# Performance work log

Measured on AMD Instinct MI355X. Metric: run time of the kernel, lower is better.

Reference implementation:

```python
import jax, jax.numpy as jnp
import numpy as np

BETA = 0.9
THRESHOLD = 1.0
SG_A = 0.5  # rectangular surrogate half-width
NUM_LAYERS = 4

@jax.custom_vjp
def spike(v):
    # heaviside fire on (mem - threshold)
    return (v > 0).astype(v.dtype)

def _spike_fwd(v):
    return spike(v), v

def _spike_bwd(v, g):
    # rectangular surrogate gradient: pass-through inside |v| <= a
    return (g * (jnp.abs(v) <= SG_A).astype(g.dtype),)

spike.defvjp(_spike_fwd, _spike_bwd)

def _lif(mem_prev, inp):
    # snntorch Leaky: reset from previous mem (detached), subtract mechanism
    reset = jax.lax.stop_gradient((mem_prev > THRESHOLD).astype(inp.dtype))
    mem = BETA * mem_prev + inp - reset * THRESHOLD
    spk = spike(mem - THRESHOLD)
    return spk, mem

def setup_inputs() -> dict:
    key = jax.random.key(0)
    k0, k1, k2 = jax.random.split(key, 3)
    L, N, OBS, H = 512, 256, 128, 512
    x = jax.random.normal(k0, (L, N, OBS), jnp.float32)
    mem0 = jnp.zeros((NUM_LAYERS + 1, N, H), jnp.float32)
    enc_W = jax.random.normal(k1, (H, OBS), jnp.float32) / np.sqrt(OBS).astype(np.float32)
    enc_b = jnp.zeros((H,), jnp.float32)
    fc_W = jax.random.normal(k2, (NUM_LAYERS, H, H), jnp.float32) / np.sqrt(H).astype(np.float32)
    fc_b = jnp.zeros((NUM_LAYERS, H), jnp.float32)
    return {"x": x, "mem0": mem0, "enc_W": enc_W, "enc_b": enc_b, "fc_W": fc_W, "fc_b": fc_b}

def reference(x, mem0, enc_W, enc_b, fc_W, fc_b):
    # x: [L, N, obs]; mem0: [num_layers+1, N, H]
    def step(mem_stack, x_t):
        spk, m0 = _lif(mem_stack[0], x_t @ enc_W.T + enc_b)  # encoder: Linear + LIF
        mems = [m0]
        for i in range(NUM_LAYERS):
            spk, m = _lif(mem_stack[i + 1], spk @ fc_W[i].T + fc_b[i])
            mems.append(m)
        return jnp.stack(mems), spk
    mem_final, outputs = jax.lax.scan(step, mem0, x)
    # outputs: [L, N, H] spikes of last layer per step; mem_final: final state list (stacked)
    return outputs, mem_final
```

## Files before the change

kernel.cpp:

```cpp
#include <hip/hip_runtime.h>

#define H 512
#define NB 256
#define OBS 128
#define LSTEPS 512
#define TB 8
#define NTB (LSTEPS / TB)
#define NPHASE (NTB + 8)
#define NWG 256
#define NTHR 512
#define NLDS_TT 5
#define PLANE (NB * H)
#define MPLANE ((size_t)TB * NB * 8)
typedef unsigned long long u64;

__global__ __launch_bounds__(256) void prep_weights(const float* __restrict__ enc_W,
                                                    const float* __restrict__ fc_W,
                                                    float* __restrict__ enc_Wt,
                                                    float* __restrict__ fc_Wt) {
    int idx = blockIdx.x * 256 + threadIdx.x;
    int stride = gridDim.x * 256;
    for (int i = idx; i < 4 * H * H; i += stride) {
        int l = i >> 18;
        int k = (i >> 9) & 511;
        int h = i & 511;
        fc_Wt[i] = fc_W[l * H * H + h * H + k];
    }
    for (int i = idx; i < OBS * H; i += stride) {
        int k = i >> 9;
        int h = i & 511;
        enc_Wt[i] = enc_W[h * OBS + k];
    }
}

__device__ __forceinline__ u64 spread2(unsigned int v) {
    u64 z = v;
    z = (z | (z << 16)) & 0x0000FFFF0000FFFFull;
    z = (z | (z << 8))  & 0x00FF00FF00FF00FFull;
    z = (z | (z << 4))  & 0x0F0F0F0F0F0F0F0Full;
    z = (z | (z << 2))  & 0x3333333333333333ull;
    z = (z | (z << 1))  & 0x5555555555555555ull;
    return z;
}
__device__ __forceinline__ u64 spread4(unsigned int v) {
    u64 z = v & 0xFFFFull;
    z = (z | (z << 24)) & 0x000000FF000000FFull;
    z = (z | (z << 12)) & 0x000F000F000F000Full;
    z = (z | (z << 6))  & 0x0303030303030303ull;
    z = (z | (z << 3))  & 0x1111111111111111ull;
    return z;
}

__global__ __launch_bounds__(NTHR, 2) void snn_persistent(
    const float* __restrict__ x,
    const float* __restrict__ mem0,
    const float* __restrict__ enc_b,
    const float* __restrict__ fc_b,
    const float* __restrict__ enc_Wt,
    const float* __restrict__ fc_Wt,
    u64* __restrict__ masks,
    int* __restrict__ bar,
    float* __restrict__ out)
{
    __shared__ float Wsh[513][64];
    __shared__ u64  Msh[TB][32][8];

    const int tid = threadIdx.x;
    const int wg  = blockIdx.x;
    const int wave = tid >> 6;
    const int lane = tid & 63;

    const int layer = wg >> 6;
    const int hs = (wg >> 3) & 7;
    const int g  = wg & 7;
    const int h0 = hs << 6;
    const int n0 = g << 5;
    const int ng = lane >> 4;
    const int hq = lane & 15;
    const int hq4 = hq << 2;
    const int nl = (wave << 2) | ng;

    const int ew  = wg >> 5;
    const int eh0 = ew << 6;
    const int en0 = (wg & 31) << 3;
    const int enl = 2 * wave + (lane >> 5);
    const int en  = en0 + enl;
    const int hp  = lane & 31;
    const int eh  = eh0 + 2 * hp;

    int* slots = bar;
    int* done  = bar + 256;
    int* rel   = bar + 288;
    const int grp = wg & 7;
    const int gidx = wg >> 3;

    const float* Wl = fc_Wt + (size_t)layer * H * H;
    #pragma unroll
    for (int i = 0; i < 16; ++i) {
        int id = tid + NTHR * i;
        int row = id >> 4, c4 = id & 15;
        *(float4*)&Wsh[row][c4 * 4] = *(const float4*)(Wl + (size_t)row * H + h0 + c4 * 4);
    }
    if (tid < 64) Wsh[512][tid] = 0.f;

    const float* WgBase = Wl + h0 + hq4;

    const float4 bfc = *(const float4*)(fc_b + layer * H + h0 + hq4);
    float4 mem_fc = *(const float4*)(mem0 + (size_t)(layer + 1) * PLANE +
                                     (size_t)(n0 + nl) * H + h0 + hq4);
    float2 be2 = make_float2(0.f, 0.f);
    float2 mem_e = make_float2(0.f, 0.f);
    if (wave < 4) {
        be2   = *(const float2*)(enc_b + eh);
        mem_e = *(const float2*)(mem0 + (size_t)en * H + eh);
    }

    __syncthreads();

    for (int p = 0; p < NPHASE; ++p) {
        const int  tb_fc  = p - 2 - 2 * layer;
        const bool fc_act = (tb_fc >= 0) && (tb_fc < NTB);
        const bool enc_act = (p < NTB);

        if (tid == 0 && p >= 2) {
            while (__hip_atomic_load(rel + grp * 32,
                                     __ATOMIC_RELAXED, __HIP_MEMORY_SCOPE_AGENT) < p - 1)
                __builtin_amdgcn_s_sleep(1);
        }
        __syncthreads();

        if (fc_act) {
            const u64* msrc = masks + ((size_t)layer * 4 + ((p + 2) & 3)) * MPLANE;
            #pragma unroll
            for (int i = 0; i < 4; ++i) {
                int id = tid + NTHR * i;
                int tt = id >> 8, n_l = (id >> 3) & 31, w = id & 7;
                u64 v = __hip_atomic_load(msrc + ((size_t)tt * NB + n0 + n_l) * 8 + w,
                                          __ATOMIC_RELAXED, __HIP_MEMORY_SCOPE_AGENT);
                Msh[tt][n_l][w] = v;
            }
        }
        __syncthreads();

        if (enc_act && wave < 4) {
            float2 ea[TB];
            #pragma unroll
            for (int tt = 0; tt < TB; ++tt) ea[tt] = make_float2(0.f, 0.f);
            const float* xbase = x + (size_t)(TB * p) * NB * OBS + (size_t)en * OBS;
            for (int k2 = 0; k2 < 64; ++k2) {
                float2 w0 = *(const float2*)(enc_Wt + (size_t)(2 * k2) * H + eh);
                float2 w1 = *(const float2*)(enc_Wt + (size_t)(2 * k2 + 1) * H + eh);
                #pragma unroll
                for (int tt = 0; tt < TB; ++tt) {
                    float2 xv = *(const float2*)(xbase + (size_t)tt * NB * OBS + 2 * k2);
                    ea[tt].x += xv.x * w0.x; ea[tt].y += xv.x * w0.y;
                    ea[tt].x += xv.y * w1.x; ea[tt].y += xv.y * w1.y;
                }
            }
            u64* edst = masks + (size_t)(0 * 4 + (p & 3)) * MPLANE;
            #pragma unroll
            for (int tt = 0; tt < TB; ++tt) {
                float m0, m1;
                {
                    float inp = ea[tt].x + be2.x; float mp = mem_e.x;
                    float reset = (mp > 1.0f) ? 1.0f : 0.0f;
                    m0 = 0.9f * mp + inp - reset; mem_e.x = m0;
                }
                {
                    float inp = ea[tt].y + be2.y; float mp = mem_e.y;
                    float reset = (mp > 1.0f) ? 1.0f : 0.0f;
                    m1 = 0.9f * mp + inp - reset; mem_e.y = m1;
                }
                u64 b0 = __ballot(m0 > 1.0f);
                u64 b1 = __ballot(m1 > 1.0f);
                unsigned int s0 = (unsigned int)(b0 >> (lane & 32));
                unsigned int s1 = (unsigned int)(b1 >> (lane & 32));
                u64 word = spread2(s0) | (spread2(s1) << 1);
                if ((lane & 31) == 0)
                    __hip_atomic_store(edst + ((size_t)tt * NB + en) * 8 + ew, word,
                                       __ATOMIC_RELAXED, __HIP_MEMORY_SCOPE_AGENT);
            }
        }

        if (fc_act) {
            float* outp = out + (size_t)(TB * tb_fc) * PLANE;
            u64* mdst = masks + ((size_t)(layer + 1) * 4 + (p & 3)) * MPLANE;

            #define LIF_PACK(TT, MNEW)                                                     \
            {                                                                              \
                if (layer < 3) {                                                           \
                    u64 B0 = __ballot(MNEW.x > 1.0f);                                      \
                    u64 B1 = __ballot(MNEW.y > 1.0f);                                      \
                    u64 B2 = __ballot(MNEW.z > 1.0f);                                      \
                    u64 B3 = __ballot(MNEW.w > 1.0f);                                      \
                    const int sh = ng << 4;                                                \
                    u64 word = spread4((unsigned int)(B0 >> sh))                           \
                             | (spread4((unsigned int)(B1 >> sh)) << 1)                    \
                             | (spread4((unsigned int)(B2 >> sh)) << 2)                    \
                             | (spread4((unsigned int)(B3 >> sh)) << 3);                   \
                    if (hq == 0)                                                           \
                        __hip_atomic_store(mdst + ((size_t)(TT) * NB + n0 + nl) * 8 + hs,  \
                                           word, __ATOMIC_RELAXED, __HIP_MEMORY_SCOPE_AGENT); \
                } else {                                                                   \
                    float4 s4;                                                             \
                    s4.x = (MNEW.x > 1.0f) ? 1.0f : 0.0f;                                  \
                    s4.y = (MNEW.y > 1.0f) ? 1.0f : 0.0f;                                  \
                    s4.z = (MNEW.z > 1.0f) ? 1.0f : 0.0f;                                  \
                    s4.w = (MNEW.w > 1.0f) ? 1.0f : 0.0f;                                  \
                    *(float4*)(outp + (size_t)(TT) * PLANE +                               \
                               (size_t)(n0 + nl) * H + h0 + hq4) = s4;                     \
                }                                                                          \
            }

            #define LIF_STEP(ACC, MNEW)                                                    \
                { float inp = ACC.x + bfc.x; float mp = mem_fc.x;                          \
                  float reset = (mp > 1.0f) ? 1.0f : 0.0f; MNEW.x = 0.9f * mp + inp - reset; } \
                { float inp = ACC.y + bfc.y; float mp = mem_fc.y;                          \
                  float reset = (mp > 1.0f) ? 1.0f : 0.0f; MNEW.y = 0.9f * mp + inp - reset; } \
                { float inp = ACC.z + bfc.z; float mp = mem_fc.z;                          \
                  float reset = (mp > 1.0f) ? 1.0f : 0.0f; MNEW.z = 0.9f * mp + inp - reset; } \
                { float inp = ACC.w + bfc.w; float mp = mem_fc.w;                          \
                  float reset = (mp > 1.0f) ? 1.0f : 0.0f; MNEW.w = 0.9f * mp + inp - reset; } \
                mem_fc = MNEW;

            #pragma unroll 1
            for (int tt = 0; tt < NLDS_TT; ++tt) {
                float4 acc = make_float4(0.f, 0.f, 0.f, 0.f);
                #pragma unroll 1
                for (int w = 0; w < 8; ++w) {
                    u64 rem = Msh[tt][nl][w];
                    if (!__any((int)(rem != 0ull))) continue;
                    const int kb = w << 6;
                    const int pop = __popcll(rem);
                    if (pop) {
                        const int nit = (pop + 1) >> 1;
                        int b0 = kb + __builtin_ctzll(rem); rem &= rem - 1;
                        int b1 = rem ? kb + __builtin_ctzll(rem) : 512; rem &= rem - 1;
                        float4 w0 = *(const float4*)&Wsh[b0][hq4];
                        float4 w1 = make_float4(0.f, 0.f, 0.f, 0.f);
                        if (b1 < 512) w1 = *(const float4*)&Wsh[b1][hq4];
                        #pragma unroll 1
                        for (int i = 1; i < nit; ++i) {
                            int c0 = kb + __builtin_ctzll(rem); rem &= rem - 1;
                            int c1 = rem ? kb + __builtin_ctzll(rem) : 512; rem &= rem - 1;
                            float4 u0 = *(const float4*)&Wsh[c0][hq4];
                            float4 u1 = make_float4(0.f, 0.f, 0.f, 0.f);
                            if (c1 < 512) u1 = *(const float4*)&Wsh[c1][hq4];
                            acc.x += w0.x; acc.y += w0.y; acc.z += w0.z; acc.w += w0.w;
                            acc.x += w1.x; acc.y += w1.y; acc.z += w1.z; acc.w += w1.w;
                            w0 = u0; w1 = u1;
                        }
                        acc.x += w0.x; acc.y += w0.y; acc.z += w0.z; acc.w += w0.w;
                        acc.x += w1.x; acc.y += w1.y; acc.z += w1.z; acc.w += w1.w;
                    }
                }
                float4 mnew;
                LIF_STEP(acc, mnew)
                LIF_PACK(tt, mnew)
            }

            #pragma unroll 1
            for (int tt = NLDS_TT; tt < TB; ++tt) {
                float4 acc = make_float4(0.f, 0.f, 0.f, 0.f);
                #pragma unroll 1
                for (int w = 0; w < 8; ++w) {
                    u64 rem = Msh[tt][nl][w];
                    if (!__any((int)(rem != 0ull))) continue;
                    const int kb = w << 6;
                    const int pop = __popcll(rem);
                    if (pop) {
                        const int nit = (pop + 1) >> 1;
                        int b0 = kb + __builtin_ctzll(rem); rem &= rem - 1;
                        int b1 = rem ? kb + __builtin_ctzll(rem) : 512; rem &= rem - 1;
                        float4 w0 = *(const float4*)(WgBase + (size_t)b0 * H);
                        float4 w1 = make_float4(0.f, 0.f, 0.f, 0.f);
                        if (b1 < 512) w1 = *(const float4*)(WgBase + (size_t)b1 * H);
                        #pragma unroll 1
                        for (int i = 1; i < nit; ++i) {
                            int c0 = kb + __builtin_ctzll(rem); rem &= rem - 1;
                            int c1 = rem ? kb + __builtin_ctzll(rem) : 512; rem &= rem - 1;
                            float4 u0 = *(const float4*)(WgBase + (size_t)c0 * H);
                            float4 u1 = make_float4(0.f, 0.f, 0.f, 0.f);
                            if (c1 < 512) u1 = *(const float4*)(WgBase + (size_t)c1 * H);
                            acc.x += w0.x; acc.y += w0.y; acc.z += w0.z; acc.w += w0.w;
                            acc.x += w1.x; acc.y += w1.y; acc.z += w1.z; acc.w += w1.w;
                            w0 = u0; w1 = u1;
                        }
                        acc.x += w0.x; acc.y += w0.y; acc.z += w0.z; acc.w += w0.w;
                        acc.x += w1.x; acc.y += w1.y; acc.z += w1.z; acc.w += w1.w;
                    }
                }
                float4 mnew;
                LIF_STEP(acc, mnew)
                LIF_PACK(tt, mnew)
            }
            #undef LIF_STEP
            #undef LIF_PACK
        }

        asm volatile("s_waitcnt vmcnt(0)" ::: "memory");
        __syncthreads();
        if (tid == 0) {
            __hip_atomic_store(slots + grp * 32 + gidx, p + 1,
                               __ATOMIC_RELAXED, __HIP_MEMORY_SCOPE_AGENT);
            if (gidx == 0 && p >= 1) {
                const int target = p;
                for (;;) {
                    int all = 1;
                    #pragma unroll
                    for (int i = 0; i < 32; ++i) {
                        int v = __hip_atomic_load(slots + grp * 32 + i,
                                                  __ATOMIC_RELAXED, __HIP_MEMORY_SCOPE_AGENT);
                        all &= (v >= target);
                    }
                    if (all) break;
                }
                __hip_atomic_store(done + grp, target,
                                   __ATOMIC_RELAXED, __HIP_MEMORY_SCOPE_AGENT);
                for (;;) {
                    int all = 1;
                    #pragma unroll
                    for (int i = 0; i < 8; ++i) {
                        int v = __hip_atomic_load(done + i,
                                                  __ATOMIC_RELAXED, __HIP_MEMORY_SCOPE_AGENT);
                        all &= (v >= target);
                    }
                    if (all) break;
                }
                __hip_atomic_store(rel + grp * 32, target,
                                   __ATOMIC_RELAXED, __HIP_MEMORY_SCOPE_AGENT);
            }
        }
    }

    float* outm = out + (size_t)LSTEPS * PLANE;
    if (wave < 4)
        *(float2*)(outm + (size_t)en * H + eh) = mem_e;
    *(float4*)(outm + (size_t)(layer + 1) * PLANE + (size_t)(n0 + nl) * H + h0 + hq4) = mem_fc;
}

extern "C" void kernel_launch(void* const* d_in, const int* in_sizes, int n_in,
                              void* d_out, int out_size, void* d_ws, size_t ws_size,
                              hipStream_t stream) {
    const float* x     = (const float*)d_in[0];
    const float* mem0  = (const float*)d_in[1];
    const float* enc_W = (const float*)d_in[2];
    const float* enc_b = (const float*)d_in[3];
    const float* fc_W  = (const float*)d_in[4];
    const float* fc_b  = (const float*)d_in[5];
    float* out = (float*)d_out;

    float* fc_Wt  = (float*)d_ws;
    float* enc_Wt = fc_Wt + 4 * H * H;
    u64*   masks  = (u64*)(enc_Wt + OBS * H);
    int*   bar    = (int*)(masks + 16 * MPLANE);

    hipMemsetAsync(bar, 0, 544 * sizeof(int), stream);
    prep_weights<<<dim3(512), dim3(256), 0, stream>>>(enc_W, fc_W, enc_Wt, fc_Wt);
    snn_persistent<<<dim3(NWG), dim3(NTHR), 0, stream>>>(
        x, mem0, enc_b, fc_b, enc_Wt, fc_Wt, masks, bar, out);
}
```

Before: 4.642 ms.

## Interleave LDS and global weight gathers across odd/even waves with 8-wide batching

Instead of every wave doing timesteps 0-4 from LDS and 5-7 from global memory, odd and even waves now swap which timesteps use LDS versus global gathers. The intent is to keep both the LDS and the global/L2 paths busy at the same time. The global gather is rewritten to issue eight independent loads per iteration, using a zero-padded row 512 in the transposed weights so that out-of-range indices need no branch. This raises the number of loads in flight and register pressure, and it grows the workspace by one row per layer.

```diff
diff --git a/kernel.cpp b/kernel.cpp
--- a/kernel.cpp
+++ b/kernel.cpp
@@ -9,7 +9,7 @@
 #define NPHASE (NTB + 8)
 #define NWG 256
 #define NTHR 512
-#define NLDS_TT 5
+#define WROWS 513
 #define PLANE (NB * H)
 #define MPLANE ((size_t)TB * NB * 8)
 typedef unsigned long long u64;
@@ -20,11 +20,11 @@
                                                     float* __restrict__ fc_Wt) {
     int idx = blockIdx.x * 256 + threadIdx.x;
     int stride = gridDim.x * 256;
-    for (int i = idx; i < 4 * H * H; i += stride) {
-        int l = i >> 18;
-        int k = (i >> 9) & 511;
+    for (int i = idx; i < 4 * WROWS * H; i += stride) {
+        int l = i / (WROWS * H);
+        int r = (i / H) % WROWS;
         int h = i & 511;
-        fc_Wt[i] = fc_W[l * H * H + h * H + k];
+        fc_Wt[i] = (r < 512) ? fc_W[l * H * H + h * H + r] : 0.0f;
     }
     for (int i = idx; i < OBS * H; i += stride) {
         int k = i >> 9;
@@ -94,7 +94,7 @@
     const int grp = wg & 7;
     const int gidx = wg >> 3;
 
-    const float* Wl = fc_Wt + (size_t)layer * H * H;
+    const float* Wl = fc_Wt + (size_t)layer * (WROWS * H);
     #pragma unroll
     for (int i = 0; i < 16; ++i) {
         int id = tid + NTHR * i;
@@ -103,7 +103,7 @@
     }
     if (tid < 64) Wsh[512][tid] = 0.f;
 
-    const float* WgBase = Wl + h0 + hq4;
+    const float* WgL = Wl + h0 + hq4;
 
     const float4 bfc = *(const float4*)(fc_b + layer * H + h0 + hq4);
     float4 mem_fc = *(const float4*)(mem0 + (size_t)(layer + 1) * PLANE +
@@ -114,6 +114,8 @@
         be2   = *(const float2*)(enc_b + eh);
         mem_e = *(const float2*)(mem0 + (size_t)en * H + eh);
     }
+
+    const bool oddw = (wave & 1) != 0;
 
     __syncthreads();
 
@@ -223,77 +225,92 @@
                   float reset = (mp > 1.0f) ? 1.0f : 0.0f; MNEW.w = 0.9f * mp + inp - reset; } \
                 mem_fc = MNEW;
 
-            #pragma unroll 1
-            for (int tt = 0; tt < NLDS_TT; ++tt) {
-                float4 acc = make_float4(0.f, 0.f, 0.f, 0.f);
-                #pragma unroll 1
-                for (int w = 0; w < 8; ++w) {
-                    u64 rem = Msh[tt][nl][w];
-                    if (!__any((int)(rem != 0ull))) continue;
-                    const int kb = w << 6;
-                    const int pop = __popcll(rem);
-                    if (pop) {
-                        const int nit = (pop + 1) >> 1;
-                        int b0 = kb + __builtin_ctzll(rem); rem &= rem - 1;
-                        int b1 = rem ? kb + __builtin_ctzll(rem) : 512; rem &= rem - 1;
-                        float4 w0 = *(const float4*)&Wsh[b0][hq4];
-                        float4 w1 = make_float4(0.f, 0.f, 0.f, 0.f);
-                        if (b1 < 512) w1 = *(const float4*)&Wsh[b1][hq4];
-                        #pragma unroll 1
-                        for (int i = 1; i < nit; ++i) {
-                            int c0 = kb + __builtin_ctzll(rem); rem &= rem - 1;
-                            int c1 = rem ? kb + __builtin_ctzll(rem) : 512; rem &= rem - 1;
-                            float4 u0 = *(const float4*)&Wsh[c0][hq4];
-                            float4 u1 = make_float4(0.f, 0.f, 0.f, 0.f);
-                            if (c1 < 512) u1 = *(const float4*)&Wsh[c1][hq4];
-                            acc.x += w0.x; acc.y += w0.y; acc.z += w0.z; acc.w += w0.w;
-                            acc.x += w1.x; acc.y += w1.y; acc.z += w1.z; acc.w += w1.w;
-                            w0 = u0; w1 = u1;
-                        }
-                        acc.x += w0.x; acc.y += w0.y; acc.z += w0.z; acc.w += w0.w;
-                        acc.x += w1.x; acc.y += w1.y; acc.z += w1.z; acc.w += w1.w;
-                    }
-                }
-                float4 mnew;
-                LIF_STEP(acc, mnew)
-                LIF_PACK(tt, mnew)
-            }
-
-            #pragma unroll 1
-            for (int tt = NLDS_TT; tt < TB; ++tt) {
-                float4 acc = make_float4(0.f, 0.f, 0.f, 0.f);
-                #pragma unroll 1
-                for (int w = 0; w < 8; ++w) {
-                    u64 rem = Msh[tt][nl][w];
-                    if (!__any((int)(rem != 0ull))) continue;
-                    const int kb = w << 6;
-                    const int pop = __popcll(rem);
-                    if (pop) {
-                        const int nit = (pop + 1) >> 1;
-                        int b0 = kb + __builtin_ctzll(rem); rem &= rem - 1;
-                        int b1 = rem ? kb + __builtin_ctzll(rem) : 512; rem &= rem - 1;
-                        float4 w0 = *(const float4*)(WgBase + (size_t)b0 * H);
-                        float4 w1 = make_float4(0.f, 0.f, 0.f, 0.f);
-                        if (b1 < 512) w1 = *(const float4*)(WgBase + (size_t)b1 * H);
-                        #pragma unroll 1
-                        for (int i = 1; i < nit; ++i) {
-                            int c0 = kb + __builtin_ctzll(rem); rem &= rem - 1;
-                            int c1 = rem ? kb + __builtin_ctzll(rem) : 512; rem &= rem - 1;
-                            float4 u0 = *(const float4*)(WgBase + (size_t)c0 * H);
-                            float4 u1 = make_float4(0.f, 0.f, 0.f, 0.f);
-                            if (c1 < 512) u1 = *(const float4*)(WgBase + (size_t)c1 * H);
-                            acc.x += w0.x; acc.y += w0.y; acc.z += w0.z; acc.w += w0.w;
-                            acc.x += w1.x; acc.y += w1.y; acc.z += w1.z; acc.w += w1.w;
-                            w0 = u0; w1 = u1;
-                        }
-                        acc.x += w0.x; acc.y += w0.y; acc.z += w0.z; acc.w += w0.w;
-                        acc.x += w1.x; acc.y += w1.y; acc.z += w1.z; acc.w += w1.w;
-                    }
-                }
-                float4 mnew;
-                LIF_STEP(acc, mnew)
-                LIF_PACK(tt, mnew)
-            }
+            #define GATHER_L(TT)                                                           \
+            {                                                                              \
+                float4 acc = make_float4(0.f, 0.f, 0.f, 0.f);                              \
+                _Pragma("unroll 1")                                                        \
+                for (int w = 0; w < 8; ++w) {                                              \
+                    u64 rem = Msh[TT][nl][w];                                              \
+                    if (!__any((int)(rem != 0ull))) continue;                              \
+                    const int kb = w << 6;                                                 \
+                    const int pop = __popcll(rem);                                         \
+                    if (pop) {                                                             \
+                        const int nit = (pop + 1) >> 1;                                    \
+                        int b0 = kb + __builtin_ctzll(rem); rem &= rem - 1;                \
+                        int b1 = rem ? kb + __builtin_ctzll(rem) : 512; rem &= rem - 1;    \
+                        float4 w0 = *(const float4*)&Wsh[b0][hq4];                         \
+                        float4 w1 = make_float4(0.f, 0.f, 0.f, 0.f);                       \
+                        if (b1 < 512) w1 = *(const float4*)&Wsh[b1][hq4];                  \
+                        _Pragma("unroll 1")                                                \
+                        for (int i = 1; i < nit; ++i) {                                    \
+                            int c0 = kb + __builtin_ctzll(rem); rem &= rem - 1;            \
+                            int c1 = rem ? kb + __builtin_ctzll(rem) : 512; rem &= rem - 1;\
+                            float4 u0 = *(const float4*)&Wsh[c0][hq4];                     \
+                            float4 u1 = make_float4(0.f, 0.f, 0.f, 0.f);                   \
+                            if (c1 < 512) u1 = *(const float4*)&Wsh[c1][hq4];              \
+                            acc.x += w0.x; acc.y += w0.y; acc.z += w0.z; acc.w += w0.w;    \
+                            acc.x += w1.x; acc.y += w1.y; acc.z += w1.z; acc.w += w1.w;    \
+                            w0 = u0; w1 = u1;                                              \
+                        }                                                                  \
+                        acc.x += w0.x; acc.y += w0.y; acc.z += w0.z; acc.w += w0.w;        \
+                        acc.x += w1.x; acc.y += w1.y; acc.z += w1.z; acc.w += w1.w;        \
+                    }                                                                      \
+                }                                                                          \
+                float4 mnew;                                                               \
+                LIF_STEP(acc, mnew)                                                        \
+                LIF_PACK(TT, mnew)                                                         \
+            }
+
+            #define GATHER_G(TT)                                                           \
+            {                                                                              \
+                float4 acc = make_float4(0.f, 0.f, 0.f, 0.f);                              \
+                _Pragma("unroll 1")                                                        \
+                for (int w = 0; w < 8; ++w) {                                              \
+                    u64 rem = Msh[TT][nl][w];                                              \
+                    const int kb = w << 6;                                                 \
+                    while (__any((int)(rem != 0ull))) {                                    \
+                        int i0 = rem ? kb + __builtin_ctzll(rem) : 512; rem &= rem - 1;    \
+                        int i1 = rem ? kb + __builtin_ctzll(rem) : 512; rem &= rem - 1;    \
+                        int i2 = rem ? kb + __builtin_ctzll(rem) : 512; rem &= rem - 1;    \
+                        int i3 = rem ? kb + __builtin_ctzll(rem) : 512; rem &= rem - 1;    \
+                        int i4 = rem ? kb + __builtin_ctzll(rem) : 512; rem &= rem - 1;    \
+                        int i5 = rem ? kb + __builtin_ctzll(rem) : 512; rem &= rem - 1;    \
+                        int i6 = rem ? kb + __builtin_ctzll(rem) : 512; rem &= rem - 1;    \
+                        int i7 = rem ? kb + __builtin_ctzll(rem) : 512; rem &= rem - 1;    \
+                        float4 v0 = *(const float4*)(WgL + (size_t)i0 * H);                \
+                        float4 v1 = *(const float4*)(WgL + (size_t)i1 * H);                \
+                        float4 v2 = *(const float4*)(WgL + (size_t)i2 * H);                \
+                        float4 v3 = *(const float4*)(WgL + (size_t)i3 * H);                \
+                        float4 v4 = *(const float4*)(WgL + (size_t)i4 * H);                \
+                        float4 v5 = *(const float4*)(WgL + (size_t)i5 * H);                \
+                        float4 v6 = *(const float4*)(WgL + (size_t)i6 * H);                \
+                        float4 v7 = *(const float4*)(WgL + (size_t)i7 * H);                \
+                        acc.x += v0.x; acc.y += v0.y; acc.z += v0.z; acc.w += v0.w;        \
+                        acc.x += v1.x; acc.y += v1.y; acc.z += v1.z; acc.w += v1.w;        \
+                        acc.x += v2.x; acc.y += v2.y; acc.z += v2.z; acc.w += v2.w;        \
+                        acc.x += v3.x; acc.y += v3.y; acc.z += v3.z; acc.w += v3.w;        \
+                        acc.x += v4.x; acc.y += v4.y; acc.z += v4.z; acc.w += v4.w;        \
+                        acc.x += v5.x; acc.y += v5.y; acc.z += v5.z; acc.w += v5.w;        \
+                        acc.x += v6.x; acc.y += v6.y; acc.z += v6.z; acc.w += v6.w;        \
+                        acc.x += v7.x; acc.y += v7.y; acc.z += v7.z; acc.w += v7.w;        \
+                    }                                                                      \
+                }                                                                          \
+                float4 mnew;                                                               \
+                LIF_STEP(acc, mnew)                                                        \
+                LIF_PACK(TT, mnew)                                                         \
+            }
+
+            if (oddw) { GATHER_G(0) } else { GATHER_L(0) }
+            if (oddw) { GATHER_G(1) } else { GATHER_L(1) }
+            if (oddw) { GATHER_G(2) } else { GATHER_L(2) }
+            GATHER_L(3)
+            GATHER_L(4)
+            if (oddw) { GATHER_L(5) } else { GATHER_G(5) }
+            if (oddw) { GATHER_L(6) } else { GATHER_G(6) }
+            if (oddw) { GATHER_L(7) } else { GATHER_G(7) }
+
+            #undef GATHER_L
+            #undef GATHER_G
             #undef LIF_STEP
             #undef LIF_PACK
         }
@@ -351,7 +368,7 @@
     float* out = (float*)d_out;
 
     float* fc_Wt  = (float*)d_ws;
-    float* enc_Wt = fc_Wt + 4 * H * H;
+    float* enc_Wt = fc_Wt + 4 * WROWS * H;
     u64*   masks  = (u64*)(enc_Wt + OBS * H);
     int*   bar    = (int*)(masks + 16 * MPLANE);
 
```

Result: slower. 4.857 ms (+4.6%).
